# Optimization experiments

Hardware: AMD Instinct MI355X
Metric: run time of the kernel (lower is better)

Reference implementation:

```python
import jax, jax.numpy as jnp
import numpy as np


def _rope(x, pos, theta):
    # x: [b, s, h, d], pos: [s] int. Standard interleaved RoPE on even/odd pairs.
    d = x.shape[-1]
    inv_freq = theta ** (-jnp.arange(0, d, 2, dtype=jnp.float32) / d)  # [d/2]
    ang = pos.astype(jnp.float32)[:, None] * inv_freq                  # [s, d/2]
    cos = jnp.cos(ang)[None, :, None, :]
    sin = jnp.sin(ang)[None, :, None, :]
    x1 = x[..., 0::2]
    x2 = x[..., 1::2]
    rot = jnp.stack([x1 * cos - x2 * sin, x1 * sin + x2 * cos], axis=-1)
    return rot.reshape(x.shape)


def setup_inputs() -> dict:
    key = jax.random.key(0)
    ks = jax.random.split(key, 5)
    b, s, d = 4, 2048, 1024
    scale = 1.0 / np.sqrt(d)
    return {
        "x": jax.random.normal(ks[0], (b, s, d), dtype=jnp.float32),
        "W_Q": jax.random.normal(ks[1], (d, d), dtype=jnp.float32) * scale,
        "W_K": jax.random.normal(ks[2], (d, d), dtype=jnp.float32) * scale,
        "W_V": jax.random.normal(ks[3], (d, d), dtype=jnp.float32) * scale,
        "W_O": jax.random.normal(ks[4], (d, d), dtype=jnp.float32) * scale,
        "token_positions": jnp.arange(s, dtype=jnp.int32),
    }


def reference(x, W_Q, W_K, W_V, W_O, token_positions):
    num_heads = 16
    theta = 10000.0
    b, s, d_model = x.shape
    d_k = d_model // num_heads

    Q = x @ W_Q.T  # [b, s, d_model]
    K = x @ W_K.T
    V = x @ W_V.T

    # split heads: last dim is [h0 | h1 | ...] so reshape to [b, s, h, d_k]
    Qh = Q.reshape(b, s, num_heads, d_k)
    Kh = K.reshape(b, s, num_heads, d_k)
    Vh = V.reshape(b, s, num_heads, d_k)

    Qh = _rope(Qh, token_positions, theta)
    Kh = _rope(Kh, token_positions, theta)

    scores = jnp.einsum("bqhd,bkhd->bhqk", Qh, Kh) / jnp.sqrt(
        jnp.asarray(d_k, dtype=x.dtype)
    )
    causal = jnp.tril(jnp.ones((s, s), dtype=bool))  # True = keep
    scores = jnp.where(causal[None, None, :, :], scores, jnp.asarray(-jnp.inf, x.dtype))
    probs = jax.nn.softmax(scores, axis=-1)

    out = jnp.einsum("bhqk,bkhd->bqhd", probs, Vh).reshape(b, s, d_model)
    return out @ W_O.T
```

## Files before the change

### kernel.cpp

```cpp
#include <hip/hip_runtime.h>
#include <hip/hip_bf16.h>
#include <type_traits>

typedef __attribute__((ext_vector_type(8))) short short8;
typedef __attribute__((ext_vector_type(4))) short s16x4;
typedef __attribute__((ext_vector_type(4))) float f32x4;
typedef unsigned short u16;
typedef unsigned int   u32;
typedef unsigned long long u64;


#if __has_builtin(__builtin_amdgcn_mfma_f32_16x16x16bf16_1k)
#define MFMA16(a, b, c) __builtin_amdgcn_mfma_f32_16x16x16bf16_1k(a, b, c, 0, 0, 0)
#define HAVE_MFMA16 1
#elif __has_builtin(__builtin_amdgcn_mfma_f32_16x16x16_bf16)
#define MFMA16(a, b, c) __builtin_amdgcn_mfma_f32_16x16x16_bf16(a, b, c, 0, 0, 0)
#define HAVE_MFMA16 1
#else
#define HAVE_MFMA16 0
#endif

static __device__ __forceinline__ u16 f2b(float f) {
  u32 u = __builtin_bit_cast(u32, f);
  u = (u + 0x7fffu + ((u >> 16) & 1u)) >> 16;
  return (u16)u;
}
static __device__ __forceinline__ float b2f(u16 h) {
  return __builtin_bit_cast(float, ((u32)h) << 16);
}
static __device__ __forceinline__ u32 pkbf(float a, float b) {
  union { __hip_bfloat162 t; u32 u; } c;
  c.t = __float22bfloat162_rn(make_float2(a, b));
  return c.u;
}

typedef __attribute__((address_space(1))) const unsigned int gas_u32;
typedef __attribute__((address_space(3))) unsigned int las_u32;
static __device__ __forceinline__ void glds16(const u16* g, u16* l) {
  __builtin_amdgcn_global_load_lds((gas_u32*)g, (las_u32*)l, 16, 0, 0);
}

__global__ __launch_bounds__(256) void cvt_all(
    const float* __restrict__ x, const float* __restrict__ wq,
    const float* __restrict__ wk, const float* __restrict__ wv,
    const float* __restrict__ wo, u16* __restrict__ xb, u16* __restrict__ wqb,
    u16* __restrict__ wkb, u16* __restrict__ wvb, u16* __restrict__ wob) {
  int u = blockIdx.x * 256 + threadIdx.x;
  if (u >= 3145728) return;
  const float* src; u16* dst; int off;
  if (u < 2097152) { src = x; dst = xb; off = u; }
  else {
    int t = u - 2097152;
    int w = t >> 18;
    off = t & 0x3FFFF;
    src = (w == 0) ? wq : (w == 1) ? wk : (w == 2) ? wv : wo;
    dst = (w == 0) ? wqb : (w == 1) ? wkb : (w == 2) ? wvb : wob;
  }
  int i = off * 4;
  float4 v = *(const float4*)(src + i);
  union { u16 us[4]; u64 ull; } o;
  o.us[0] = f2b(v.x); o.us[1] = f2b(v.y); o.us[2] = f2b(v.z); o.us[3] = f2b(v.w);
  *(u64*)(dst + i) = o.ull;
}

template <typename OT>
static __device__ __forceinline__ void gemm_body(const u16* __restrict__ A,
                                                 const u16* __restrict__ B,
                                                 OT* __restrict__ C,
                                                 int m0, int n0) {
  __shared__ u16 As[4096];
  __shared__ u16 Bs[4096];

  const int tid  = threadIdx.x;
  const int lane = tid & 63;
  const int wv   = tid >> 6;
  const int quad = lane >> 4;
  const int cc   = lane & 15;
  const int wr   = wv >> 1;
  const int wc   = wv & 1;

  f32x4 acc[4][4];
#pragma unroll
  for (int i = 0; i < 4; i++)
#pragma unroll
    for (int j = 0; j < 4; j++) acc[i][j] = (f32x4){0.f, 0.f, 0.f, 0.f};

  const int p0 = wv * 128 + lane;
  const int p1 = p0 + 64;
  const int r0 = p0 >> 2, g0 = (p0 & 3) ^ (r0 & 3);
  const int r1 = p1 >> 2, g1 = (p1 & 3) ^ (r1 & 3);
  const u16* gA0 = A + (size_t)(m0 + r0) * 1024 + g0 * 8;
  const u16* gA1 = A + (size_t)(m0 + r1) * 1024 + g1 * 8;
  const u16* gB0 = B + (size_t)(n0 + r0) * 1024 + g0 * 8;
  const u16* gB1 = B + (size_t)(n0 + r1) * 1024 + g1 * 8;
  u16* lA = As + wv * 1024;
  u16* lB = Bs + wv * 1024;

  for (int k0 = 0; k0 < 1024; k0 += 32) {
    __syncthreads();
    glds16(gA0 + k0, lA);
    glds16(gA1 + k0, lA + 512);
    glds16(gB0 + k0, lB);
    glds16(gB1 + k0, lB + 512);
    __syncthreads();

    short8 af[4], bf[4];
#pragma unroll
    for (int mt = 0; mt < 4; mt++) {
      int ra = wr * 64 + mt * 16 + cc;
      af[mt] = *(const short8*)&As[ra * 32 + ((quad ^ (ra & 3)) * 8)];
    }
#pragma unroll
    for (int nt = 0; nt < 4; nt++) {
      int rb = wc * 64 + nt * 16 + cc;
      bf[nt] = *(const short8*)&Bs[rb * 32 + ((quad ^ (rb & 3)) * 8)];
    }
#pragma unroll
    for (int mt = 0; mt < 4; mt++)
#pragma unroll
      for (int nt = 0; nt < 4; nt++)
        acc[mt][nt] = __builtin_amdgcn_mfma_f32_16x16x32_bf16(af[mt], bf[nt], acc[mt][nt], 0, 0, 0);
  }

#pragma unroll
  for (int mt = 0; mt < 4; mt++)
#pragma unroll
    for (int nt = 0; nt < 4; nt++)
#pragma unroll
      for (int r = 0; r < 4; r++) {
        int row = m0 + wr * 64 + mt * 16 + quad * 4 + r;
        int col = n0 + wc * 64 + nt * 16 + cc;
        if constexpr (std::is_same_v<OT, float>)
          C[(size_t)row * 1024 + col] = acc[mt][nt][r];
        else
          C[(size_t)row * 1024 + col] = f2b(acc[mt][nt][r]);
      }
}

__global__ __launch_bounds__(256) void gemm_qkv(const u16* __restrict__ A,
                                                const u16* __restrict__ Bq,
                                                const u16* __restrict__ Bk,
                                                const u16* __restrict__ Bv,
                                                u16* __restrict__ Q,
                                                u16* __restrict__ K,
                                                u16* __restrict__ V) {
  int sel = blockIdx.x >> 3;
  const u16* B = (sel == 0) ? Bq : (sel == 1) ? Bk : Bv;
  u16* C = (sel == 0) ? Q : (sel == 1) ? K : V;
  gemm_body<u16>(A, B, C, blockIdx.y * 128, (blockIdx.x & 7) * 128);
}

__global__ __launch_bounds__(256) void gemm_out(const u16* __restrict__ A,
                                                const u16* __restrict__ B,
                                                float* __restrict__ C) {
  gemm_body<float>(A, B, C, blockIdx.y * 128, blockIdx.x * 128);
}

__global__ __launch_bounds__(256) void rope_kernel(u16* __restrict__ Q,
                                                   u16* __restrict__ K,
                                                   const int* __restrict__ pos) {
  u16* T = blockIdx.y ? K : Q;
  const float sc = blockIdx.y ? 1.0f : 0.18033688011112042f;
  int idx = blockIdx.x * 256 + threadIdx.x;
  int row = idx >> 9;
  int p   = idx & 511;
  int i   = p & 31;
  int col = (p >> 5) * 64 + 2 * i;
  int s   = row & 2047;
  float ps  = (float)pos[s];
  float inv = exp2f(-(float)i * 0.41524101186092033f);
  float ang = ps * inv;
  float sn, cs;
  sincosf(ang, &sn, &cs);
  u32 v = *(u32*)(T + (size_t)row * 1024 + col);
  float x1 = b2f((u16)(v & 0xffffu));
  float x2 = b2f((u16)(v >> 16));
  float y1 = (x1 * cs - x2 * sn) * sc;
  float y2 = (x1 * sn + x2 * cs) * sc;
  *(u32*)(T + (size_t)row * 1024 + col) = (u32)f2b(y1) | ((u32)f2b(y2) << 16);
}

__global__ __launch_bounds__(256) void transpose_v(const u16* __restrict__ V,
                                                   u16* __restrict__ Vt) {
  __shared__ u16 t[64][65];
  int s0 = blockIdx.x * 64;
  int bh = blockIdx.y;
  int b = bh >> 4, h = bh & 15;
  int tid = threadIdx.x;
  int r = tid >> 2, ch = (tid & 3) * 16;
  const u16* src = V + (size_t)(b * 2048 + s0 + r) * 1024 + h * 64 + ch;
  union { uint4 v[2]; u16 us[16]; } tmp;
  tmp.v[0] = *(const uint4*)src;
  tmp.v[1] = *(const uint4*)(src + 8);
#pragma unroll
  for (int j = 0; j < 16; j++) t[r][ch + j] = tmp.us[j];
  __syncthreads();
  union { uint4 v[2]; u16 us[16]; } o;
#pragma unroll
  for (int j = 0; j < 16; j++) o.us[j] = t[ch + j][r];
  u16* dst = Vt + (size_t)(bh * 64 + r) * 2048 + s0 + ch;
  *(uint4*)dst = o.v[0];
  *(uint4*)(dst + 8) = o.v[1];
}


#define S_STEP(MT, SV)                                                     \
  do {                                                                     \
    __builtin_amdgcn_s_setprio(1);                                         \
    _Pragma("unroll")                                                      \
    for (int nt = 0; nt < 8; ++nt) {                                       \
      const int rbase = (nt * 16 + cc) * 64;                               \
      short8 bk0 = *(const short8*)&Ks[cur][rbase + pk0];                  \
      short8 bk1 = *(const short8*)&Ks[cur][rbase + (pk0 ^ 32)];           \
      f32x4 z = (f32x4){0.f, 0.f, 0.f, 0.f};                               \
      z = __builtin_amdgcn_mfma_f32_16x16x32_bf16(bk0, qf[MT][0], z, 0, 0, 0); \
      SV[nt] = __builtin_amdgcn_mfma_f32_16x16x32_bf16(bk1, qf[MT][1], z, 0, 0, 0); \
    }                                                                      \
    __builtin_amdgcn_s_setprio(0);                                         \
  } while (0)

#define MASK_STEP(MT, SV)                                                  \
  do {                                                                     \
    const int qg = q0 + wv * 32 + MT * 16 + cc;                            \
    const int kb = kt * 128 + quad * 4;                                    \
    _Pragma("unroll")                                                      \
    for (int nt = 0; nt < 8; ++nt)                                         \
      _Pragma("unroll")                                                    \
      for (int r = 0; r < 4; ++r)                                          \
        if (kb + nt * 16 + r > qg) SV[nt][r] = -3.0e38f;                   \
  } while (0)

#define MAXRED_STEP(MT, SV)                                                \
  do {                                                                     \
    float mx = fmaxf(fmaxf(SV[0][0], SV[0][1]), fmaxf(SV[0][2], SV[0][3]));\
    _Pragma("unroll")                                                      \
    for (int nt = 1; nt < 8; ++nt)                                         \
      mx = fmaxf(mx, fmaxf(fmaxf(SV[nt][0], SV[nt][1]),                    \
                           fmaxf(SV[nt][2], SV[nt][3])));                  \
    mx = fmaxf(mx, __shfl_xor(mx, 16));                                    \
    mx = fmaxf(mx, __shfl_xor(mx, 32));                                    \
    if (!__all(mx <= m_i[MT] + 11.0f)) {                                   \
      const float mn = fmaxf(m_i[MT], mx);                                 \
      const float al = exp2f(m_i[MT] - mn);                                \
      m_i[MT] = mn;                                                        \
      l_i[MT] *= al;                                                       \
      f32x4 al4;                                                           \
      _Pragma("unroll")                                                    \
      for (int r = 0; r < 4; ++r) al4[r] = __shfl(al, quad * 4 + r);       \
      _Pragma("unroll")                                                    \
      for (int nt = 0; nt < 4; ++nt) o_acc[MT][nt] *= al4;                 \
    }                                                                      \
  } while (0)

#if HAVE_MFMA16
#define EXPPV_STEP(MT, SV)                                                 \
  do {                                                                     \
    const float mu = m_i[MT];                                              \
    float ps = 0.f;                                                        \
    __builtin_amdgcn_s_setprio(1);                                         \
    _Pragma("unroll")                                                      \
    for (int kk = 0; kk < 8; ++kk) {                                       \
      float e0 = exp2f(SV[kk][0] - mu);                                    \
      float e1 = exp2f(SV[kk][1] - mu);                                    \
      float e2 = exp2f(SV[kk][2] - mu);                                    \
      float e3 = exp2f(SV[kk][3] - mu);                                    \
      ps += (e0 + e1) + (e2 + e3);                                         \
      union { u32 w[2]; s16x4 v; } pu;                                     \
      pu.w[0] = pkbf(e0, e1);                                              \
      pu.w[1] = pkbf(e2, e3);                                              \
      const int pos = (kk * 2 + (quad >> 1) + cc) & 15;                    \
      _Pragma("unroll")                                                    \
      for (int nt = 0; nt < 4; ++nt) {                                     \
        s16x4 bv = *(const s16x4*)&Vs[(nt * 16 + cc) * 128 + pos * 8 + (quad & 1) * 4]; \
        o_acc[MT][nt] = MFMA16(pu.v, bv, o_acc[MT][nt]);                   \
      }                                                                    \
    }                                                                      \
    __builtin_amdgcn_s_setprio(0);                                         \
    l_i[MT] += ps;                                                         \
  } while (0)
#else
#define EXPPV_STEP(MT, SV)                                                 \
  do {                                                                     \
    const float mu = m_i[MT];                                              \
    float ps = 0.f;                                                        \
    s16x4 pf[8];                                                           \
    _Pragma("unroll")                                                      \
    for (int nt = 0; nt < 8; ++nt) {                                       \
      float e0 = exp2f(SV[nt][0] - mu);                                    \
      float e1 = exp2f(SV[nt][1] - mu);                                    \
      float e2 = exp2f(SV[nt][2] - mu);                                    \
      float e3 = exp2f(SV[nt][3] - mu);                                    \
      ps += (e0 + e1) + (e2 + e3);                                         \
      union { u32 w[2]; s16x4 v; } pu;                                     \
      pu.w[0] = pkbf(e0, e1);                                              \
      pu.w[1] = pkbf(e2, e3);                                              \
      pf[nt] = pu.v;                                                       \
    }                                                                      \
    l_i[MT] += ps;                                                         \
    _Pragma("unroll")                                                      \
    for (int nt = 0; nt < 8; ++nt) {                                       \
      union { s16x4 v; u64 ull; } pu2; pu2.v = pf[nt];                     \
      *(u64*)&Ps[(wv * 16 + cc) * 136 + nt * 16 + quad * 4] = pu2.ull;     \
    }                                                                      \
    short8 pa[4];                                                          \
    _Pragma("unroll")                                                      \
    for (int ks = 0; ks < 4; ++ks)                                         \
      pa[ks] = *(const short8*)&Ps[(wv * 16 + cc) * 136 + ks * 32 + quad * 8];\
    _Pragma("unroll")                                                      \
    for (int nt = 0; nt < 4; ++nt) {                                       \
      const int rv = (nt * 16 + cc) * 128;                                 \
      _Pragma("unroll")                                                    \
      for (int ks = 0; ks < 4; ++ks) {                                     \
        const int pos = (ks * 4 + quad + cc) & 15;                         \
        short8 bv = *(const short8*)&Vs[rv + pos * 8];                     \
        o_acc[MT][nt] = __builtin_amdgcn_mfma_f32_16x16x32_bf16(pa[ks], bv, o_acc[MT][nt], 0, 0, 0); \
      }                                                                    \
    }                                                                      \
  } while (0)
#endif

__global__ __launch_bounds__(256) void attn_kernel(const u16* __restrict__ Q,
                                                   const u16* __restrict__ K,
                                                   const u16* __restrict__ Vt,
                                                   u16* __restrict__ O) {
  __shared__ u16 Ks[2][8192];
  __shared__ u16 Vs[8192];
#if !HAVE_MFMA16
  __shared__ u16 Ps[4 * 16 * 136];
#endif

  const int bh = blockIdx.x;
  const int qt = 15 - blockIdx.y;
  const int b = bh >> 4, h = bh & 15;
  const int tid  = threadIdx.x;
  const int lane = tid & 63;
  const int wv   = tid >> 6;
  const int quad = lane >> 4;
  const int cc   = lane & 15;
  const int q0   = qt * 128;

  short8 qf[2][2];
#pragma unroll
  for (int mt = 0; mt < 2; mt++) {
    const u16* qp = Q + (size_t)(b * 2048 + q0 + wv * 32 + mt * 16 + cc) * 1024 + h * 64;
    qf[mt][0] = *(const short8*)(qp + quad * 8);
    qf[mt][1] = *(const short8*)(qp + 32 + quad * 8);
  }

  f32x4 o_acc[2][4];
  float m_i[2] = {-3.0e38f, -3.0e38f}, l_i[2] = {0.f, 0.f};
#pragma unroll
  for (int mt = 0; mt < 2; mt++)
#pragma unroll
    for (int nt = 0; nt < 4; nt++) o_acc[mt][nt] = (f32x4){0.f, 0.f, 0.f, 0.f};

  const u16* Kp = K + ((size_t)(b * 2048) + wv * 32 + (lane >> 3)) * 1024 + h * 64 +
                  (((lane & 7) ^ (lane >> 3)) * 8);
  const u16* Vp[4];
#pragma unroll
  for (int j = 0; j < 4; j++) {
    int rl = wv * 16 + j * 4 + (lane >> 4);
    int g  = ((lane & 15) - rl) & 15;
    Vp[j] = Vt + ((size_t)(bh * 64) + rl) * 2048 + g * 8;
  }

  const int nkt = qt + 1;
  const int pk0 = (quad ^ (cc & 7)) * 8;

#pragma unroll
  for (int j = 0; j < 4; j++)
    glds16(Kp + j * 8192, &Ks[0][wv * 2048 + j * 512]);
  __syncthreads();

  for (int kt = 0; kt < nkt; ++kt) {
    const int cur = kt & 1;

#pragma unroll
    for (int j = 0; j < 4; j++)
      glds16(Vp[j] + kt * 128, Vs + wv * 2048 + j * 512);
    if (kt + 1 < nkt) {
#pragma unroll
      for (int j = 0; j < 4; j++)
        glds16(Kp + (size_t)(kt + 1) * 131072 + j * 8192,
               &Ks[cur ^ 1][wv * 2048 + j * 512]);
    }

    const bool diag = (kt == qt);

    {
      f32x4 s[8];
      S_STEP(0, s);
      if (diag) MASK_STEP(0, s);
      MAXRED_STEP(0, s);

      __syncthreads();

      EXPPV_STEP(0, s);
    }

    {
      f32x4 s[8];
      S_STEP(1, s);
      if (diag) MASK_STEP(1, s);
      MAXRED_STEP(1, s);
      EXPPV_STEP(1, s);
    }

    __syncthreads();
  }

#pragma unroll
  for (int mt = 0; mt < 2; ++mt) {
    float l = l_i[mt];
    l += __shfl_xor(l, 16);
    l += __shfl_xor(l, 32);
    const float linv = 1.0f / l;
    f32x4 li4;
#pragma unroll
    for (int r = 0; r < 4; ++r) li4[r] = __shfl(linv, quad * 4 + r);
    const int rowb = b * 2048 + q0 + wv * 32 + mt * 16 + quad * 4;
#pragma unroll
    for (int nt = 0; nt < 4; ++nt)
#pragma unroll
      for (int r = 0; r < 4; ++r)
        O[(size_t)(rowb + r) * 1024 + h * 64 + nt * 16 + cc] = f2b(o_acc[mt][nt][r] * li4[r]);
  }
}

extern "C" void kernel_launch(void* const* d_in, const int* in_sizes, int n_in,
                              void* d_out, int out_size, void* d_ws, size_t ws_size,
                              hipStream_t stream) {
  const float* x  = (const float*)d_in[0];
  const float* wq = (const float*)d_in[1];
  const float* wk = (const float*)d_in[2];
  const float* wv = (const float*)d_in[3];
  const float* wo = (const float*)d_in[4];
  const int* pos  = (const int*)d_in[5];
  float* out = (float*)d_out;

  char* ws = (char*)d_ws;
  u16* xb  = (u16*)(ws);
  u16* vt  = (u16*)(ws);
  u16* wqb = (u16*)(ws + (16ull << 20));
  u16* wkb = (u16*)(ws + (18ull << 20));
  u16* wvb = (u16*)(ws + (20ull << 20));
  u16* wob = (u16*)(ws + (22ull << 20));
  u16* Qb  = (u16*)(ws + (24ull << 20));
  u16* Kb  = (u16*)(ws + (40ull << 20));
  u16* Vb  = (u16*)(ws + (56ull << 20));
  u16* aO  = Vb;

  cvt_all<<<12288, 256, 0, stream>>>(x, wq, wk, wv, wo, xb, wqb, wkb, wvb, wob);
  gemm_qkv<<<dim3(24, 64), 256, 0, stream>>>(xb, wqb, wkb, wvb, Qb, Kb, Vb);
  rope_kernel<<<dim3(16384, 2), 256, 0, stream>>>(Qb, Kb, pos);
  transpose_v<<<dim3(32, 64), 256, 0, stream>>>(Vb, vt);
  attn_kernel<<<dim3(64, 16), 256, 0, stream>>>(Qb, Kb, vt, aO);
  gemm_out<<<dim3(8, 64), 256, 0, stream>>>(aO, wob, out);
}
```

Measured before the change: 305.3 us.

## Fuse V transpose into QKV GEMM epilogue and bound attention occupancy

The QKV GEMM now writes the V projection directly in transposed [b, d, s] layout, packing four consecutive sequence rows into one 64-bit store, so the separate transpose_v kernel and its extra round trip through global memory are removed. The workspace is remapped so the attention output reuses the xb region and Vt gets its own slot. Attention also gains a launch-bounds minimum of three blocks per CU, which can limit registers and cause spills. The transposed epilogue stores are strided by 2048 elements across lanes, which may be less coalesced than the original row-major writes.

```diff
diff --git a/kernel.cpp b/kernel.cpp
--- a/kernel.cpp
+++ b/kernel.cpp
@@ -63,7 +63,7 @@
   *(u64*)(dst + i) = o.ull;
 }
 
-template <typename OT>
+template <typename OT, int TM>
 static __device__ __forceinline__ void gemm_body(const u16* __restrict__ A,
                                                  const u16* __restrict__ B,
                                                  OT* __restrict__ C,
@@ -125,16 +125,28 @@
 #pragma unroll
   for (int mt = 0; mt < 4; mt++)
 #pragma unroll
-    for (int nt = 0; nt < 4; nt++)
-#pragma unroll
-      for (int r = 0; r < 4; r++) {
-        int row = m0 + wr * 64 + mt * 16 + quad * 4 + r;
-        int col = n0 + wc * 64 + nt * 16 + cc;
-        if constexpr (std::is_same_v<OT, float>)
-          C[(size_t)row * 1024 + col] = acc[mt][nt][r];
-        else
-          C[(size_t)row * 1024 + col] = f2b(acc[mt][nt][r]);
+    for (int nt = 0; nt < 4; nt++) {
+      if constexpr (TM == 2) {
+        const int col = n0 + wc * 64 + nt * 16 + cc;
+        const int rowbase = m0 + wr * 64 + mt * 16 + quad * 4;
+        const int bsel = rowbase >> 11;
+        const int s0 = rowbase & 2047;
+        union { u16 us[4]; u64 ull; } o;
+#pragma unroll
+        for (int r = 0; r < 4; r++) o.us[r] = f2b(acc[mt][nt][r]);
+        *(u64*)&C[((size_t)(bsel * 1024 + col)) * 2048 + s0] = o.ull;
+      } else {
+#pragma unroll
+        for (int r = 0; r < 4; r++) {
+          int row = m0 + wr * 64 + mt * 16 + quad * 4 + r;
+          int col = n0 + wc * 64 + nt * 16 + cc;
+          if constexpr (TM == 0)
+            C[(size_t)row * 1024 + col] = acc[mt][nt][r];
+          else
+            C[(size_t)row * 1024 + col] = f2b(acc[mt][nt][r]);
+        }
       }
+    }
 }
 
 __global__ __launch_bounds__(256) void gemm_qkv(const u16* __restrict__ A,
@@ -143,17 +155,18 @@
                                                 const u16* __restrict__ Bv,
                                                 u16* __restrict__ Q,
                                                 u16* __restrict__ K,
-                                                u16* __restrict__ V) {
+                                                u16* __restrict__ Vt) {
   int sel = blockIdx.x >> 3;
-  const u16* B = (sel == 0) ? Bq : (sel == 1) ? Bk : Bv;
-  u16* C = (sel == 0) ? Q : (sel == 1) ? K : V;
-  gemm_body<u16>(A, B, C, blockIdx.y * 128, (blockIdx.x & 7) * 128);
+  int m0 = blockIdx.y * 128, n0 = (blockIdx.x & 7) * 128;
+  if (sel == 0)      gemm_body<u16, 1>(A, Bq, Q,  m0, n0);
+  else if (sel == 1) gemm_body<u16, 1>(A, Bk, K,  m0, n0);
+  else               gemm_body<u16, 2>(A, Bv, Vt, m0, n0);
 }
 
 __global__ __launch_bounds__(256) void gemm_out(const u16* __restrict__ A,
                                                 const u16* __restrict__ B,
                                                 float* __restrict__ C) {
-  gemm_body<float>(A, B, C, blockIdx.y * 128, blockIdx.x * 128);
+  gemm_body<float, 0>(A, B, C, blockIdx.y * 128, blockIdx.x * 128);
 }
 
 __global__ __launch_bounds__(256) void rope_kernel(u16* __restrict__ Q,
@@ -180,29 +193,6 @@
   *(u32*)(T + (size_t)row * 1024 + col) = (u32)f2b(y1) | ((u32)f2b(y2) << 16);
 }
 
-__global__ __launch_bounds__(256) void transpose_v(const u16* __restrict__ V,
-                                                   u16* __restrict__ Vt) {
-  __shared__ u16 t[64][65];
-  int s0 = blockIdx.x * 64;
-  int bh = blockIdx.y;
-  int b = bh >> 4, h = bh & 15;
-  int tid = threadIdx.x;
-  int r = tid >> 2, ch = (tid & 3) * 16;
-  const u16* src = V + (size_t)(b * 2048 + s0 + r) * 1024 + h * 64 + ch;
-  union { uint4 v[2]; u16 us[16]; } tmp;
-  tmp.v[0] = *(const uint4*)src;
-  tmp.v[1] = *(const uint4*)(src + 8);
-#pragma unroll
-  for (int j = 0; j < 16; j++) t[r][ch + j] = tmp.us[j];
-  __syncthreads();
-  union { uint4 v[2]; u16 us[16]; } o;
-#pragma unroll
-  for (int j = 0; j < 16; j++) o.us[j] = t[ch + j][r];
-  u16* dst = Vt + (size_t)(bh * 64 + r) * 2048 + s0 + ch;
-  *(uint4*)dst = o.v[0];
-  *(uint4*)(dst + 8) = o.v[1];
-}
-
 
 #define S_STEP(MT, SV)                                                     \
   do {                                                                     \
@@ -319,10 +309,10 @@
   } while (0)
 #endif
 
-__global__ __launch_bounds__(256) void attn_kernel(const u16* __restrict__ Q,
-                                                   const u16* __restrict__ K,
-                                                   const u16* __restrict__ Vt,
-                                                   u16* __restrict__ O) {
+__global__ __launch_bounds__(256, 3) void attn_kernel(const u16* __restrict__ Q,
+                                                      const u16* __restrict__ K,
+                                                      const u16* __restrict__ Vt,
+                                                      u16* __restrict__ O) {
   __shared__ u16 Ks[2][8192];
   __shared__ u16 Vs[8192];
 #if !HAVE_MFMA16
@@ -440,20 +430,18 @@
 
   char* ws = (char*)d_ws;
   u16* xb  = (u16*)(ws);
-  u16* vt  = (u16*)(ws);
+  u16* aO  = (u16*)(ws);
   u16* wqb = (u16*)(ws + (16ull << 20));
   u16* wkb = (u16*)(ws + (18ull << 20));
   u16* wvb = (u16*)(ws + (20ull << 20));
   u16* wob = (u16*)(ws + (22ull << 20));
   u16* Qb  = (u16*)(ws + (24ull << 20));
   u16* Kb  = (u16*)(ws + (40ull << 20));
-  u16* Vb  = (u16*)(ws + (56ull << 20));
-  u16* aO  = Vb;
+  u16* vt  = (u16*)(ws + (56ull << 20));
 
   cvt_all<<<12288, 256, 0, stream>>>(x, wq, wk, wv, wo, xb, wqb, wkb, wvb, wob);
-  gemm_qkv<<<dim3(24, 64), 256, 0, stream>>>(xb, wqb, wkb, wvb, Qb, Kb, Vb);
+  gemm_qkv<<<dim3(24, 64), 256, 0, stream>>>(xb, wqb, wkb, wvb, Qb, Kb, vt);
   rope_kernel<<<dim3(16384, 2), 256, 0, stream>>>(Qb, Kb, pos);
-  transpose_v<<<dim3(32, 64), 256, 0, stream>>>(Vb, vt);
   attn_kernel<<<dim3(64, 16), 256, 0, stream>>>(Qb, Kb, vt, aO);
   gemm_out<<<dim3(8, 64), 256, 0, stream>>>(aO, wob, out);
 }
```

After: 287.9 us. 1.06x faster.
